# Kernel tuning notes

Hardware: AMD Instinct MI355X
Metric: run time of the kernel (lower is better)

The kernel has to match this reference:

```python
import jax, jax.numpy as jnp
import numpy as np

N, K, C, L = 8192, 12, 128, 6
FF = 4 * C
SIG_LO, SIG_HI = 1.0, 5.0
BOX = 25.0

TRI_NAMES = ("ln_g", "ln_b", "Wa", "ba", "Wga", "bga", "Wb", "bb", "Wgb", "bgb",
             "lno_g", "lno_b", "Wo", "bo", "Wgo", "bgo")
FFN_NAMES = ("ln_g", "ln_b", "W1", "b1", "W2", "b2")


def _ln(x, g, b, eps=1e-5):
    m = jnp.mean(x, axis=-1, keepdims=True)
    v = jnp.mean((x - m) ** 2, axis=-1, keepdims=True)
    return (x - m) * jax.lax.rsqrt(v + eps) * g + b


def _knn_embed(coords):
    # pairwise distances -> k smallest (self included), Gaussian RBF bank over C sigmas
    d2 = jnp.sum((coords[:, None, :] - coords[None, :, :]) ** 2, axis=-1)  # [N,N]
    dist = jnp.sqrt(jnp.maximum(d2, 0.0))
    neg_d, nbr = jax.lax.top_k(-dist, K)                      # [N,K]
    k_dist = -neg_d
    sig = jnp.linspace(SIG_LO, SIG_HI, C)                     # [C]
    g = jnp.exp(-(k_dist[..., None] ** 2) / (2.0 * sig ** 2))  # [N,K,C]
    vals = jnp.where(g > 0.1, g, 0.0)                         # threshold as in repo
    vals = jnp.where(jnp.isnan(vals), 0.0, vals)
    return nbr, vals


def _transpose_vals(v, nbr):
    # sparse rowcol_transpose: value of edge (j,i) aligned to slot of edge (i,j); 0 if absent
    n = nbr.shape[0]
    nn = nbr[nbr]                                   # [N,K,K]: neighbor lists of each neighbor j
    eq = nn == jnp.arange(n)[:, None, None]         # slot where j lists i back
    pos = jnp.argmax(eq, axis=-1)                   # [N,K]
    found = jnp.any(eq, axis=-1)                    # [N,K]
    tv = v[nbr, pos]                                # [N,K,C] value at edge (j,i)
    return jnp.where(found[..., None], tv, jnp.zeros_like(tv))


def _tri_update(v, nbr, p, incoming):
    x = _ln(v, p["ln_g"], p["ln_b"])
    a = jax.nn.sigmoid(x @ p["Wga"] + p["bga"]) * (x @ p["Wa"] + p["ba"])
    b = jax.nn.sigmoid(x @ p["Wgb"] + p["bgb"]) * (x @ p["Wb"] + p["bb"])
    if incoming:  # column/incoming update operates on transposed edges
        a = _transpose_vals(a, nbr)
        b = _transpose_vals(b, nbr)
    # sparse triangle multiplicative update over KNN neighbor slots
    k = jnp.einsum('ntc,nmtc->nmc', a, b[nbr])      # [N,K,C]
    o = _ln(k, p["lno_g"], p["lno_b"]) @ p["Wo"] + p["bo"]
    return jax.nn.sigmoid(x @ p["Wgo"] + p["bgo"]) * o


def _ffn(v, p):
    x = _ln(v, p["ln_g"], p["ln_b"])
    return jax.nn.gelu(x @ p["W1"] + p["b1"], approximate=False) @ p["W2"] + p["b2"]


def _forward(coords, tri, ffn, dec_W, dec_b):
    nbr, v = _knn_embed(coords)
    v = jax.lax.stop_gradient(v)  # embedding runs under torch.no_grad in the original

    def step(v, lp):
        tp, fp = lp
        p_row = {n: t[0] for n, t in zip(TRI_NAMES, tp)}
        p_col = {n: t[1] for n, t in zip(TRI_NAMES, tp)}
        v = v + _tri_update(v, nbr, p_row, False)   # row (outgoing) update
        v = v + _tri_update(v, nbr, p_col, True)    # col (incoming) update
        v = v + _ffn(v, dict(zip(FFN_NAMES, fp)))
        return v, None

    v, _ = jax.lax.scan(jax.checkpoint(step), v, (tri, ffn))
    s = v + _transpose_vals(v, nbr)                 # sparse_operation(edge, edge^T, op='sum')
    e = s @ dec_W + dec_b                           # [N,K,1] decode
    rows = jnp.repeat(jnp.arange(N), K)
    dense = jnp.zeros((N, N, e.shape[-1]), e.dtype)
    dense = dense.at[rows, nbr.reshape(-1)].add(e.reshape(-1, e.shape[-1]))
    return dense                                    # [N,N,1] like .to_dense()


def setup_inputs() -> dict:
    key = jax.random.key(0)
    ks = jax.random.split(key, 8)
    coords = jax.random.uniform(ks[0], (N, 3), jnp.float32) * BOX

    def lin(k, fin, fout, pre=()):
        kw, _ = jax.random.split(k)
        W = jax.random.normal(kw, pre + (fin, fout), jnp.float32) / np.sqrt(fin).astype(np.float32)
        b = jnp.zeros(pre + (fout,), jnp.float32)
        return W, b

    inp = {"coords": coords}
    k_iter = iter(jax.random.split(ks[1], 16))
    pre = (L, 2)
    inp["tri_ln_g"] = jnp.ones(pre + (C,), jnp.float32)
    inp["tri_ln_b"] = jnp.zeros(pre + (C,), jnp.float32)
    for nm in ("a", "ga", "b", "gb", "o", "go"):
        W, b = lin(next(k_iter), C, C, pre)
        inp[f"tri_W{nm}"] = W
        inp[f"tri_b{nm}"] = b
    inp["tri_lno_g"] = jnp.ones(pre + (C,), jnp.float32)
    inp["tri_lno_b"] = jnp.zeros(pre + (C,), jnp.float32)
    inp["ffn_ln_g"] = jnp.ones((L, C), jnp.float32)
    inp["ffn_ln_b"] = jnp.zeros((L, C), jnp.float32)
    inp["ffn_W1"], inp["ffn_b1"] = lin(next(k_iter), C, FF, (L,))
    inp["ffn_W2"], inp["ffn_b2"] = lin(next(k_iter), FF, C, (L,))
    inp["dec_W"], inp["dec_b"] = lin(next(k_iter), C, 1)
    return inp


def reference(coords, tri_ln_g, tri_ln_b, tri_Wa, tri_ba, tri_Wga, tri_bga,
              tri_Wb, tri_bb, tri_Wgb, tri_bgb, tri_lno_g, tri_lno_b,
              tri_Wo, tri_bo, tri_Wgo, tri_bgo,
              ffn_ln_g, ffn_ln_b, ffn_W1, ffn_b1, ffn_W2, ffn_b2,
              dec_W, dec_b):
    tri = (tri_ln_g, tri_ln_b, tri_Wa, tri_ba, tri_Wga, tri_bga,
           tri_Wb, tri_bb, tri_Wgb, tri_bgb, tri_lno_g, tri_lno_b,
           tri_Wo, tri_bo, tri_Wgo, tri_bgo)
    ffn = (ffn_ln_g, ffn_ln_b, ffn_W1, ffn_b1, ffn_W2, ffn_b2)
    return _forward(coords, tri, ffn, dec_W, dec_b)
```

## Files before the change

kernel.cpp:

```cpp
#include <hip/hip_runtime.h>
#include <hip/hip_bf16.h>
#include <stdint.h>
#include <stddef.h>

#define NPTS 8192
#define KNN  12
#define CH   128
#define FFD  512
#define MEDGE (NPTS * KNN)

typedef __attribute__((ext_vector_type(8))) _Float16 half8;
typedef __attribute__((ext_vector_type(4))) _Float16 half4;
typedef __attribute__((ext_vector_type(4))) float f32x4;

__device__ __forceinline__ float wave_sum(float v) {
#pragma unroll
  for (int off = 32; off > 0; off >>= 1) v += __shfl_xor(v, off, 64);
  return v;
}
__device__ __forceinline__ float sigm_(float x) { return 1.0f / (1.0f + expf(-x)); }
__device__ __forceinline__ float gelu_(float x) { return 0.5f * x * (1.0f + erff(x * 0.7071067811865475f)); }

__global__ __launch_bounds__(256)
void prep_coords(const float* __restrict__ c, float4* __restrict__ c4)
{
  int i = blockIdx.x * 256 + threadIdx.x;
  if (i < NPTS) c4[i] = make_float4(c[3 * i], c[3 * i + 1], c[3 * i + 2], 0.0f);
}

struct SwzArgs {
  const float* src[8];
  _Float16* dst[8];
  int K[8], N[8], B[8], perB[8];
};

__global__ __launch_bounds__(256)
void prep_weights_swz(SwzArgs sa)
{
  int g = blockIdx.y;
  int idx = blockIdx.x * 256 + threadIdx.x;
  int perB = sa.perB[g];
  if (idx >= sa.B[g] * perB) return;
  int K = sa.K[g], N = sa.N[g];
  int b = idx / perB;
  int c = idx - b * perB;
  int l16 = c & 15;
  int quad = (c >> 4) & 3;
  int rest = c >> 6;
  int kts = K >> 5;
  int kt = rest % kts;
  int mt = rest / kts;
  const float* sp = sa.src[g] + ((size_t)b * K + kt * 32 + quad * 8) * N + mt * 16 + l16;
  _Float16* dp = sa.dst[g] + ((size_t)b * perB + c) * 8;
#pragma unroll
  for (int e = 0; e < 8; ++e) dp[e] = (_Float16)sp[(size_t)e * N];
}

#define KNN_CAP 2048

__global__ __launch_bounds__(256)
void knn_embed(const float4* __restrict__ coords4, const float* __restrict__ lng,
               const float* __restrict__ lnb, int* __restrict__ nbr,
               float* __restrict__ v0, _Float16* __restrict__ xln)
{
#pragma clang fp contract(off)
  __shared__ unsigned long long buf[KNN_CAP];
  __shared__ unsigned long long sel[KNN];
  __shared__ int cnt_s;
  const int i = blockIdx.x;
  const int tid = threadIdx.x;
  const int lane = tid & 63;
  const int wv = tid >> 6;
  const float4 ci = coords4[i];

  float T2 = 9.0f;
  int cnt;
  while (true) {
    if (tid == 0) cnt_s = 0;
    __syncthreads();
    for (int j = tid; j < NPTS; j += 256) {
      float4 cj = coords4[j];
      float dx = ci.x - cj.x;
      float dy = ci.y - cj.y;
      float dz = ci.z - cj.z;
      float d2 = dx * dx + dy * dy + dz * dz;
      if (d2 < T2) {
        unsigned long long key =
            (((unsigned long long)__float_as_uint(sqrtf(d2))) << 32) | (unsigned int)j;
        int idx = atomicAdd(&cnt_s, 1);
        if (idx < KNN_CAP) buf[idx] = key;
      }
    }
    __syncthreads();
    cnt = cnt_s;
    if (cnt >= KNN) break;
    T2 *= 4.0f;
    __syncthreads();
  }
  if (cnt > KNN_CAP) cnt = KNN_CAP;

  if (wv == 0) {
    unsigned long long best[KNN];
#pragma unroll
    for (int q = 0; q < KNN; ++q) best[q] = ~0ULL;
    for (int p2 = lane; p2 < cnt; p2 += 64) {
      unsigned long long key = buf[p2];
      if (key < best[KNN - 1]) {
        best[KNN - 1] = key;
#pragma unroll
        for (int q = KNN - 2; q >= 0; --q) {
          if (best[q + 1] < best[q]) { unsigned long long t = best[q]; best[q] = best[q + 1]; best[q + 1] = t; }
        }
      }
    }
    int p = 0;
    for (int r = 0; r < KNN; ++r) {
      unsigned long long c = ~0ULL;
#pragma unroll
      for (int q = 0; q < KNN; ++q) if (q == p) c = best[q];
      unsigned long long m = c;
#pragma unroll
      for (int off = 32; off > 0; off >>= 1) {
        unsigned long long o = __shfl_xor(m, off, 64);
        if (o < m) m = o;
      }
      if (c == m) ++p;
      if (lane == 0) sel[r] = m;
    }
  }
  __syncthreads();
  if (tid < KNN) nbr[i * KNN + tid] = (int)(unsigned int)(sel[tid] & 0xFFFFFFFFULL);

  float g1 = lng[lane], g2 = lng[lane + 64];
  float bb1 = lnb[lane], bb2 = lnb[lane + 64];
  for (int k = wv * 3; k < wv * 3 + 3; ++k) {
    float d = __uint_as_float((unsigned int)(sel[k] >> 32));
    float sig1 = (float)(1.0 + 4.0 * (double)lane / 127.0);
    float sig2 = (float)(1.0 + 4.0 * (double)(lane + 64) / 127.0);
    float e1 = expf((-(d * d)) / (2.0f * sig1 * sig1));
    float e2 = expf((-(d * d)) / (2.0f * sig2 * sig2));
    float v1 = (e1 > 0.1f) ? e1 : 0.0f;
    float v2 = (e2 > 0.1f) ? e2 : 0.0f;
    size_t off = (size_t)(i * KNN + k) * CH;
    v0[off + lane] = v1;
    v0[off + lane + 64] = v2;
    float m = wave_sum(v1 + v2) * (1.0f / 128.0f);
    float d1 = v1 - m, d2 = v2 - m;
    float var = wave_sum(d1 * d1 + d2 * d2) * (1.0f / 128.0f);
    float rs = 1.0f / sqrtf(var + 1e-5f);
    xln[off + lane]      = (_Float16)(d1 * rs * g1 + bb1);
    xln[off + lane + 64] = (_Float16)(d2 * rs * g2 + bb2);
  }
}

__global__ __launch_bounds__(256)
void build_tidx(const int* __restrict__ nbr, int* __restrict__ tidx)
{
  int e = blockIdx.x * 256 + threadIdx.x;
  if (e >= MEDGE) return;
  int i = e / KNN;
  int j = nbr[e];
  int res = -1;
#pragma unroll
  for (int t = 0; t < KNN; ++t) {
    if (nbr[j * KNN + t] == i) { res = j * KNN + t; break; }
  }
  tidx[e] = res;
}

__global__ __launch_bounds__(256)
void gemm_ab_go(const _Float16* __restrict__ xln,
                const _Float16* __restrict__ wa,  const float* __restrict__ ba,
                const _Float16* __restrict__ wga, const float* __restrict__ bga,
                const _Float16* __restrict__ wb,  const float* __restrict__ bb,
                const _Float16* __restrict__ wgb, const float* __restrict__ bgb,
                const _Float16* __restrict__ wgo, const float* __restrict__ bgo,
                _Float16* __restrict__ aout, _Float16* __restrict__ bout,
                _Float16* __restrict__ gobout)
{
  const int lane = threadIdx.x & 63;
  const int quad = lane >> 4;
  const int l16 = lane & 15;
  const int gw = blockIdx.x * 4 + (threadIdx.x >> 6);
  const int base = gw * 32;
  const int chbase = quad * 16 + l16;

  half8 xf[2][4];
#pragma unroll
  for (int rt = 0; rt < 2; ++rt)
#pragma unroll
    for (int kt = 0; kt < 4; ++kt)
      xf[rt][kt] = *(const half8*)(xln + (size_t)(base + rt * 16 + l16) * CH + kt * 32 + quad * 8);

  const half8* WA  = (const half8*)wa;
  const half8* WGA = (const half8*)wga;
  const half8* WB  = (const half8*)wb;
  const half8* WGB = (const half8*)wgb;
  const half8* WGO = (const half8*)wgo;

#pragma unroll
  for (int mt = 0; mt < 8; ++mt) {
    f32x4 aA[2], aGA[2], aB[2], aGB[2], aGO[2];
    const f32x4 z = {0.f, 0.f, 0.f, 0.f};
#pragma unroll
    for (int rt = 0; rt < 2; ++rt) { aA[rt] = z; aGA[rt] = z; aB[rt] = z; aGB[rt] = z; aGO[rt] = z; }
#pragma unroll
    for (int kt = 0; kt < 4; ++kt) {
      int ch = (mt * 4 + kt) * 64 + chbase;
      half8 wfa = WA[ch], wfga = WGA[ch], wfb = WB[ch], wfgb = WGB[ch], wfgo = WGO[ch];
#pragma unroll
      for (int rt = 0; rt < 2; ++rt) {
        aA[rt]  = __builtin_amdgcn_mfma_f32_16x16x32_f16(wfa,  xf[rt][kt], aA[rt], 0, 0, 0);
        aGA[rt] = __builtin_amdgcn_mfma_f32_16x16x32_f16(wfga, xf[rt][kt], aGA[rt], 0, 0, 0);
        aB[rt]  = __builtin_amdgcn_mfma_f32_16x16x32_f16(wfb,  xf[rt][kt], aB[rt], 0, 0, 0);
        aGB[rt] = __builtin_amdgcn_mfma_f32_16x16x32_f16(wfgb, xf[rt][kt], aGB[rt], 0, 0, 0);
        aGO[rt] = __builtin_amdgcn_mfma_f32_16x16x32_f16(wfgo, xf[rt][kt], aGO[rt], 0, 0, 0);
      }
    }
    f32x4 bva  = *(const f32x4*)(ba  + mt * 16 + quad * 4);
    f32x4 bvga = *(const f32x4*)(bga + mt * 16 + quad * 4);
    f32x4 bvb  = *(const f32x4*)(bb  + mt * 16 + quad * 4);
    f32x4 bvgb = *(const f32x4*)(bgb + mt * 16 + quad * 4);
    f32x4 bvgo = *(const f32x4*)(bgo + mt * 16 + quad * 4);
#pragma unroll
    for (int rt = 0; rt < 2; ++rt) {
      half4 av, bv, gv;
#pragma unroll
      for (int r = 0; r < 4; ++r) {
        av[r] = (_Float16)(sigm_(aGA[rt][r] + bvga[r]) * (aA[rt][r] + bva[r]));
        bv[r] = (_Float16)(sigm_(aGB[rt][r] + bvgb[r]) * (aB[rt][r] + bvb[r]));
        gv[r] = (_Float16)(sigm_(aGO[rt][r] + bvgo[r]));
      }
      size_t off = (size_t)(base + rt * 16 + l16) * CH + mt * 16 + quad * 4;
      *(half4*)(aout + off) = av;
      *(half4*)(bout + off) = bv;
      *(half4*)(gobout + off) = gv;
    }
  }
}

__global__ __launch_bounds__(192)
void tri_einsum_ln(const _Float16* __restrict__ a, const _Float16* __restrict__ b,
                   const int* __restrict__ nbr, const int* __restrict__ tidx,
                   const float* __restrict__ lng, const float* __restrict__ lnb,
                   _Float16* __restrict__ kout, int incoming)
{
  __shared__ float As[KNN][CH];
  __shared__ int bidx[KNN][KNN];
  __shared__ int nbr_s[KNN];
  const int n = blockIdx.x;
  const int tid = threadIdx.x;
  if (tid < KNN) nbr_s[tid] = nbr[n * KNN + tid];
  __syncthreads();
  if (tid < KNN * KNN) {
    int m = tid / KNN, t = tid - m * KNN;
    int j = nbr_s[m];
    bidx[m][t] = incoming ? tidx[j * KNN + t] : (j * KNN + t);
  }
  for (int idx = tid; idx < KNN * CH; idx += 192) {
    int t = idx >> 7, c = idx & 127;
    float av;
    if (incoming) {
      int ti = tidx[n * KNN + t];
      av = (ti >= 0) ? (float)(a[(size_t)ti * CH + c]) : 0.0f;
    } else {
      av = (float)(a[(size_t)(n * KNN + t) * CH + c]);
    }
    As[t][c] = av;
  }
  __syncthreads();

  const int m = tid >> 4;
  const int c8 = (tid & 15) * 8;
  float acc[8];
#pragma unroll
  for (int r = 0; r < 8; ++r) acc[r] = 0.0f;
#pragma unroll
  for (int t = 0; t < KNN; ++t) {
    int bi = bidx[m][t];
    if (bi >= 0) {
      half8 bv = *(const half8*)(b + (size_t)bi * CH + c8);
      f32x4 a0 = *(const f32x4*)&As[t][c8];
      f32x4 a1 = *(const f32x4*)&As[t][c8 + 4];
#pragma unroll
      for (int r = 0; r < 4; ++r) acc[r] += a0[r] * (float)bv[r];
#pragma unroll
      for (int r = 0; r < 4; ++r) acc[4 + r] += a1[r] * (float)bv[4 + r];
    }
  }
  float s = 0.0f, sq = 0.0f;
#pragma unroll
  for (int r = 0; r < 8; ++r) { s += acc[r]; sq += acc[r] * acc[r]; }
#pragma unroll
  for (int off = 1; off < 16; off <<= 1) {
    s += __shfl_xor(s, off, 64);
    sq += __shfl_xor(sq, off, 64);
  }
  float mean = s * (1.0f / 128.0f);
  float var = sq * (1.0f / 128.0f) - mean * mean;
  if (var < 0.0f) var = 0.0f;
  float rs = 1.0f / sqrtf(var + 1e-5f);
  half8 o;
#pragma unroll
  for (int r = 0; r < 8; ++r)
    o[r] = (_Float16)((acc[r] - mean) * rs * lng[c8 + r] + lnb[c8 + r]);
  *(half8*)(kout + (size_t)(n * KNN + m) * CH + c8) = o;
}

__global__ __launch_bounds__(256)
void og_gemm(const _Float16* __restrict__ kln,
             const _Float16* __restrict__ wo,  const float* __restrict__ bo,
             const _Float16* __restrict__ gob, float* __restrict__ v,
             const float* __restrict__ nlng, const float* __restrict__ nlnb,
             _Float16* __restrict__ xlnN)
{
  const int lane = threadIdx.x & 63;
  const int quad = lane >> 4;
  const int l16 = lane & 15;
  const int gw = blockIdx.x * 4 + (threadIdx.x >> 6);
  const int base = gw * 16;
  const int chbase = quad * 16 + l16;
  const size_t rowOff = (size_t)(base + l16) * CH;

  half8 kf[4];
#pragma unroll
  for (int kt = 0; kt < 4; ++kt)
    kf[kt] = *(const half8*)(kln + rowOff + kt * 32 + quad * 8);

  const half8* WO = (const half8*)wo;
  f32x4 vn[8];
  float s = 0.0f, sq = 0.0f;
#pragma unroll
  for (int mt = 0; mt < 8; ++mt) {
    f32x4 acc = {0.f, 0.f, 0.f, 0.f};
#pragma unroll
    for (int kt = 0; kt < 4; ++kt)
      acc = __builtin_amdgcn_mfma_f32_16x16x32_f16(WO[(mt * 4 + kt) * 64 + chbase], kf[kt], acc, 0, 0, 0);
    half4 g4 = *(const half4*)(gob + rowOff + mt * 16 + quad * 4);
    f32x4 bo4 = *(const f32x4*)(bo + mt * 16 + quad * 4);
    f32x4 vv = *(const f32x4*)(v + rowOff + mt * 16 + quad * 4);
#pragma unroll
    for (int r = 0; r < 4; ++r) {
      float nv = vv[r] + (float)g4[r] * (acc[r] + bo4[r]);
      vn[mt][r] = nv;
      s += nv;
      sq += nv * nv;
    }
    *(f32x4*)(v + rowOff + mt * 16 + quad * 4) = vn[mt];
  }
  s  += __shfl_xor(s, 16, 64);  s  += __shfl_xor(s, 32, 64);
  sq += __shfl_xor(sq, 16, 64); sq += __shfl_xor(sq, 32, 64);
  float mean = s * (1.0f / 128.0f);
  float var = sq * (1.0f / 128.0f) - mean * mean;
  if (var < 0.0f) var = 0.0f;
  float rs = 1.0f / sqrtf(var + 1e-5f);
#pragma unroll
  for (int mt = 0; mt < 8; ++mt) {
    f32x4 g4 = *(const f32x4*)(nlng + mt * 16 + quad * 4);
    f32x4 b4 = *(const f32x4*)(nlnb + mt * 16 + quad * 4);
    half4 o;
#pragma unroll
    for (int r = 0; r < 4; ++r)
      o[r] = (_Float16)((vn[mt][r] - mean) * rs * g4[r] + b4[r]);
    *(half4*)(xlnN + rowOff + mt * 16 + quad * 4) = o;
  }
}

#define HADDR(row, ch) ((((row) * 64 + ((ch) ^ ((row) & 7)))) * 8)

__global__ __launch_bounds__(256)
void ffn_fused(const _Float16* __restrict__ xln,
               const _Float16* __restrict__ w1, const float* __restrict__ b1,
               const _Float16* __restrict__ w2, const float* __restrict__ b2,
               float* __restrict__ v,
               const float* __restrict__ nlng, const float* __restrict__ nlnb,
               _Float16* __restrict__ xlnN)
{
  __shared__ alignas(16) _Float16 hlds[32 * FFD];
  __shared__ float part[32][4][2];
  const int tid = threadIdx.x;
  const int lane = tid & 63;
  const int w = tid >> 6;
  const int quad = lane >> 4;
  const int l16 = lane & 15;
  const int rowBase = blockIdx.x * 32;
  const int chbase = quad * 16 + l16;

  half8 xf[2][4];
#pragma unroll
  for (int rt = 0; rt < 2; ++rt)
#pragma unroll
    for (int kt = 0; kt < 4; ++kt)
      xf[rt][kt] = *(const half8*)(xln + (size_t)(rowBase + rt * 16 + l16) * CH + kt * 32 + quad * 8);

  const half8* W1 = (const half8*)w1;
#pragma unroll
  for (int mt = 0; mt < 8; ++mt) {
    int mtg = w * 8 + mt;
    f32x4 acc[2];
    const f32x4 z = {0.f, 0.f, 0.f, 0.f};
    acc[0] = z; acc[1] = z;
#pragma unroll
    for (int kt = 0; kt < 4; ++kt) {
      half8 wf = W1[(mtg * 4 + kt) * 64 + chbase];
#pragma unroll
      for (int rt = 0; rt < 2; ++rt)
        acc[rt] = __builtin_amdgcn_mfma_f32_16x16x32_f16(wf, xf[rt][kt], acc[rt], 0, 0, 0);
    }
    f32x4 bv = *(const f32x4*)(b1 + mtg * 16 + quad * 4);
    int ch = mtg * 2 + (quad >> 1);
    int sub = (quad & 1) * 4;
#pragma unroll
    for (int rt = 0; rt < 2; ++rt) {
      int row = rt * 16 + l16;
      half4 hh;
#pragma unroll
      for (int r = 0; r < 4; ++r)
        hh[r] = (_Float16)(gelu_(acc[rt][r] + bv[r]));
      *(half4*)&hlds[HADDR(row, ch) + sub] = hh;
    }
  }
  __syncthreads();

  const half8* W2 = (const half8*)w2;
  f32x4 vn2[2][2];
  float s2[2] = {0.f, 0.f}, q2[2] = {0.f, 0.f};
#pragma unroll
  for (int m2 = 0; m2 < 2; ++m2) {
    int mt = w * 2 + m2;
    f32x4 accA[2], accB[2];
    const f32x4 z = {0.f, 0.f, 0.f, 0.f};
    accA[0] = z; accA[1] = z; accB[0] = z; accB[1] = z;
#pragma unroll
    for (int kt = 0; kt < 16; kt += 2) {
      half8 wf0 = W2[(mt * 16 + kt) * 64 + chbase];
      half8 wf1 = W2[(mt * 16 + kt + 1) * 64 + chbase];
#pragma unroll
      for (int rt = 0; rt < 2; ++rt) {
        int row = rt * 16 + l16;
        half8 hf0 = *(const half8*)&hlds[HADDR(row, kt * 4 + quad)];
        half8 hf1 = *(const half8*)&hlds[HADDR(row, (kt + 1) * 4 + quad)];
        accA[rt] = __builtin_amdgcn_mfma_f32_16x16x32_f16(wf0, hf0, accA[rt], 0, 0, 0);
        accB[rt] = __builtin_amdgcn_mfma_f32_16x16x32_f16(wf1, hf1, accB[rt], 0, 0, 0);
      }
    }
    f32x4 bv = *(const f32x4*)(b2 + mt * 16 + quad * 4);
#pragma unroll
    for (int rt = 0; rt < 2; ++rt) {
      size_t off = (size_t)(rowBase + rt * 16 + l16) * CH + mt * 16 + quad * 4;
      f32x4 vv = *(const f32x4*)(v + off);
#pragma unroll
      for (int r = 0; r < 4; ++r) {
        float nv = vv[r] + accA[rt][r] + accB[rt][r] + bv[r];
        vn2[m2][rt][r] = nv;
        s2[rt] += nv;
        q2[rt] += nv * nv;
      }
      *(f32x4*)(v + off) = vn2[m2][rt];
    }
  }
#pragma unroll
  for (int rt = 0; rt < 2; ++rt) {
    float ss = s2[rt], qq = q2[rt];
    ss += __shfl_xor(ss, 16, 64); ss += __shfl_xor(ss, 32, 64);
    qq += __shfl_xor(qq, 16, 64); qq += __shfl_xor(qq, 32, 64);
    if (quad == 0) { part[rt * 16 + l16][w][0] = ss; part[rt * 16 + l16][w][1] = qq; }
  }
  __syncthreads();
#pragma unroll
  for (int rt = 0; rt < 2; ++rt) {
    int row = rt * 16 + l16;
    float su = part[row][0][0] + part[row][1][0] + part[row][2][0] + part[row][3][0];
    float qu = part[row][0][1] + part[row][1][1] + part[row][2][1] + part[row][3][1];
    float mean = su * (1.0f / 128.0f);
    float var = qu * (1.0f / 128.0f) - mean * mean;
    if (var < 0.0f) var = 0.0f;
    float rs = 1.0f / sqrtf(var + 1e-5f);
#pragma unroll
    for (int m2 = 0; m2 < 2; ++m2) {
      int mt = w * 2 + m2;
      f32x4 g4 = *(const f32x4*)(nlng + mt * 16 + quad * 4);
      f32x4 b4 = *(const f32x4*)(nlnb + mt * 16 + quad * 4);
      half4 o;
#pragma unroll
      for (int r = 0; r < 4; ++r)
        o[r] = (_Float16)((vn2[m2][rt][r] - mean) * rs * g4[r] + b4[r]);
      *(half4*)(xlnN + (size_t)(rowBase + row) * CH + mt * 16 + quad * 4) = o;
    }
  }
}

__global__ __launch_bounds__(256)
void decode_row(const float* __restrict__ vin, const int* __restrict__ tidx,
                const int* __restrict__ nbr, const float* __restrict__ decW,
                const float* __restrict__ decB, float* __restrict__ out)
{
  __shared__ float ev[KNN];
  __shared__ int nbr_s[KNN];
  const int n = blockIdx.x;
  const int tid = threadIdx.x;
  const int lane = tid & 63;
  const int w = tid >> 6;
  if (tid < KNN) nbr_s[tid] = nbr[n * KNN + tid];
  float dw1 = decW[lane], dw2 = decW[lane + 64];
  for (int k = w; k < KNN; k += 4) {
    int e = n * KNN + k;
    int ti = tidx[e];
    float s1 = vin[(size_t)e * CH + lane];
    float s2 = vin[(size_t)e * CH + 64 + lane];
    if (ti >= 0) {
      s1 += vin[(size_t)ti * CH + lane];
      s2 += vin[(size_t)ti * CH + 64 + lane];
    }
    float tot = wave_sum(s1 * dw1 + s2 * dw2);
    if (lane == 0) ev[k] = tot + decB[0];
  }
  __syncthreads();
  float4 z = make_float4(0.f, 0.f, 0.f, 0.f);
  float4* row = (float4*)(out + (size_t)n * NPTS);
  for (int idx = tid; idx < NPTS / 4; idx += 256) row[idx] = z;
  __syncthreads();
  if (tid < KNN) out[(size_t)n * NPTS + nbr_s[tid]] = ev[tid];
}

extern "C" void kernel_launch(void* const* d_in, const int* in_sizes, int n_in,
                              void* d_out, int out_size, void* d_ws, size_t ws_size,
                              hipStream_t stream)
{
  (void)in_sizes; (void)n_in; (void)out_size; (void)ws_size;
  const float* coords  = (const float*)d_in[0];
  const float* t_ln_g  = (const float*)d_in[1];
  const float* t_ln_b  = (const float*)d_in[2];
  const float* t_Wa    = (const float*)d_in[3];
  const float* t_ba    = (const float*)d_in[4];
  const float* t_Wga   = (const float*)d_in[5];
  const float* t_bga   = (const float*)d_in[6];
  const float* t_Wb    = (const float*)d_in[7];
  const float* t_bb    = (const float*)d_in[8];
  const float* t_Wgb   = (const float*)d_in[9];
  const float* t_bgb   = (const float*)d_in[10];
  const float* t_Wo    = (const float*)d_in[11];
  const float* t_bo    = (const float*)d_in[12];
  const float* t_Wgo   = (const float*)d_in[13];
  const float* t_bgo   = (const float*)d_in[14];
  const float* t_lno_g = (const float*)d_in[15];
  const float* t_lno_b = (const float*)d_in[16];
  const float* f_ln_g  = (const float*)d_in[17];
  const float* f_ln_b  = (const float*)d_in[18];
  const float* f_W1    = (const float*)d_in[19];
  const float* f_b1    = (const float*)d_in[20];
  const float* f_W2    = (const float*)d_in[21];
  const float* f_b2    = (const float*)d_in[22];
  const float* dec_W   = (const float*)d_in[23];
  const float* dec_b   = (const float*)d_in[24];

  const size_t NKC = (size_t)MEDGE * CH;
  char* ws = (char*)d_ws;
  float* v        = (float*)(ws);
  _Float16* kln   = (_Float16*)(ws + NKC * 4);
  _Float16* gx    = (_Float16*)(ws + NKC * 6);
  int* nbr        = (int*)(ws + NKC * 8);
  int* tidx       = (int*)(ws + NKC * 8 + (size_t)MEDGE * 4);
  float4* coords4 = (float4*)(ws + NKC * 8 + (size_t)MEDGE * 8);
  _Float16* wbase = (_Float16*)(ws + NKC * 8 + (size_t)MEDGE * 8 + NPTS * 16);
  const size_t TRIH = (size_t)12 * 2048 * 8;
  _Float16* wA  = wbase;
  _Float16* wGA = wA  + TRIH;
  _Float16* wB  = wGA + TRIH;
  _Float16* wGB = wB  + TRIH;
  _Float16* wGO = wGB + TRIH;
  _Float16* wO  = wGO + TRIH;
  _Float16* w1  = wO  + TRIH;
  _Float16* w2  = w1  + (size_t)6 * 8192 * 8;

  _Float16* abuf = (_Float16*)d_out;
  _Float16* bbuf = abuf + NKC;

  prep_coords<<<32, 256, 0, stream>>>(coords, coords4);

  SwzArgs sa;
  sa.src[0] = t_Wa;  sa.dst[0] = wA;  sa.K[0] = CH;  sa.N[0] = CH;  sa.B[0] = 12; sa.perB[0] = 2048;
  sa.src[1] = t_Wga; sa.dst[1] = wGA; sa.K[1] = CH;  sa.N[1] = CH;  sa.B[1] = 12; sa.perB[1] = 2048;
  sa.src[2] = t_Wb;  sa.dst[2] = wB;  sa.K[2] = CH;  sa.N[2] = CH;  sa.B[2] = 12; sa.perB[2] = 2048;
  sa.src[3] = t_Wgb; sa.dst[3] = wGB; sa.K[3] = CH;  sa.N[3] = CH;  sa.B[3] = 12; sa.perB[3] = 2048;
  sa.src[4] = t_Wgo; sa.dst[4] = wGO; sa.K[4] = CH;  sa.N[4] = CH;  sa.B[4] = 12; sa.perB[4] = 2048;
  sa.src[5] = t_Wo;  sa.dst[5] = wO;  sa.K[5] = CH;  sa.N[5] = CH;  sa.B[5] = 12; sa.perB[5] = 2048;
  sa.src[6] = f_W1;  sa.dst[6] = w1;  sa.K[6] = CH;  sa.N[6] = FFD; sa.B[6] = 6;  sa.perB[6] = 8192;
  sa.src[7] = f_W2;  sa.dst[7] = w2;  sa.K[7] = FFD; sa.N[7] = CH;  sa.B[7] = 6;  sa.perB[7] = 8192;
  dim3 pgrid(192, 8);
  prep_weights_swz<<<pgrid, 256, 0, stream>>>(sa);

  knn_embed<<<NPTS, 256, 0, stream>>>(coords4, t_ln_g, t_ln_b, nbr, v, gx);
  build_tidx<<<MEDGE / 256, 256, 0, stream>>>(nbr, tidx);

  const size_t WS = (size_t)2048 * 8;
  gemm_ab_go<<<MEDGE / 128, 256, 0, stream>>>(gx,
      wA, t_ba, wGA, t_bga, wB, t_bb, wGB, t_bgb, wGO, t_bgo,
      abuf, bbuf, gx);

  for (int l = 0; l < 6; ++l) {
    int s0 = 2 * l, s1 = 2 * l + 1, s2 = 2 * l + 2;
    tri_einsum_ln<<<NPTS, 192, 0, stream>>>(abuf, bbuf, nbr, tidx,
        t_lno_g + s0 * CH, t_lno_b + s0 * CH, kln, 0);
    og_gemm<<<MEDGE / 64, 256, 0, stream>>>(kln,
        wO + s0 * WS, t_bo + s0 * CH, gx, v,
        t_ln_g + s1 * CH, t_ln_b + s1 * CH, gx);
    gemm_ab_go<<<MEDGE / 128, 256, 0, stream>>>(gx,
        wA + s1 * WS, t_ba + s1 * CH, wGA + s1 * WS, t_bga + s1 * CH,
        wB + s1 * WS, t_bb + s1 * CH, wGB + s1 * WS, t_bgb + s1 * CH,
        wGO + s1 * WS, t_bgo + s1 * CH,
        abuf, bbuf, gx);
    tri_einsum_ln<<<NPTS, 192, 0, stream>>>(abuf, bbuf, nbr, tidx,
        t_lno_g + s1 * CH, t_lno_b + s1 * CH, kln, 1);
    og_gemm<<<MEDGE / 64, 256, 0, stream>>>(kln,
        wO + s1 * WS, t_bo + s1 * CH, gx, v,
        f_ln_g + l * CH, f_ln_b + l * CH, gx);
    const float* ng = (l < 5) ? (t_ln_g + s2 * CH) : t_ln_g;
    const float* nb = (l < 5) ? (t_ln_b + s2 * CH) : t_ln_b;
    ffn_fused<<<MEDGE / 32, 256, 0, stream>>>(gx,
        w1 + (size_t)l * 8192 * 8, f_b1 + l * FFD,
        w2 + (size_t)l * 8192 * 8, f_b2 + l * CH,
        v, ng, nb, gx);
    if (l < 5) {
      gemm_ab_go<<<MEDGE / 128, 256, 0, stream>>>(gx,
          wA + s2 * WS, t_ba + s2 * CH, wGA + s2 * WS, t_bga + s2 * CH,
          wB + s2 * WS, t_bb + s2 * CH, wGB + s2 * WS, t_bgb + s2 * CH,
          wGO + s2 * WS, t_bgo + s2 * CH,
          abuf, bbuf, gx);
    }
  }

  decode_row<<<NPTS, 256, 0, stream>>>(v, tidx, nbr, dec_W, dec_b, (float*)d_out);
}
```

Measured before the change: 2.611 ms.

## Fuse triangle einsum+LN with output gated GEMM via LDS staging

Merges the sparse triangle einsum/LayerNorm kernel with the output projection/gating GEMM. Each block now handles 4 points (48 edge rows) and keeps the normalized triangle result in LDS instead of writing it to and rereading it from a global buffer. The A operand is staged in LDS as fp16 with 16-byte vector loads instead of scalar fp32. The trade-off is that 192-thread blocks give 3 MFMA waves for the GEMM stage instead of 4 per block, and more LDS per block may reduce occupancy.

Result: no change. 2.563 ms (-1.8%).

```diff
diff --git a/kernel.cpp b/kernel.cpp
--- a/kernel.cpp
+++ b/kernel.cpp
@@ -240,92 +240,97 @@
 }
 
 __global__ __launch_bounds__(192)
-void tri_einsum_ln(const _Float16* __restrict__ a, const _Float16* __restrict__ b,
-                   const int* __restrict__ nbr, const int* __restrict__ tidx,
-                   const float* __restrict__ lng, const float* __restrict__ lnb,
-                   _Float16* __restrict__ kout, int incoming)
-{
-  __shared__ float As[KNN][CH];
-  __shared__ int bidx[KNN][KNN];
-  __shared__ int nbr_s[KNN];
-  const int n = blockIdx.x;
+void tri_og(const _Float16* __restrict__ a, const _Float16* __restrict__ b,
+            const int* __restrict__ nbr, const int* __restrict__ tidx,
+            const float* __restrict__ lng, const float* __restrict__ lnb,
+            const _Float16* __restrict__ wo, const float* __restrict__ bo,
+            const _Float16* __restrict__ gob, float* __restrict__ v,
+            const float* __restrict__ nlng, const float* __restrict__ nlnb,
+            _Float16* __restrict__ xlnN, int incoming)
+{
+  __shared__ alignas(16) _Float16 As[48][136];
+  __shared__ alignas(16) _Float16 klds[48][136];
+  __shared__ int bidx[4][KNN][KNN];
+  __shared__ int nbr_s[4][KNN];
+  const int n0 = blockIdx.x * 4;
   const int tid = threadIdx.x;
-  if (tid < KNN) nbr_s[tid] = nbr[n * KNN + tid];
-  __syncthreads();
-  if (tid < KNN * KNN) {
-    int m = tid / KNN, t = tid - m * KNN;
-    int j = nbr_s[m];
-    bidx[m][t] = incoming ? tidx[j * KNN + t] : (j * KNN + t);
-  }
-  for (int idx = tid; idx < KNN * CH; idx += 192) {
-    int t = idx >> 7, c = idx & 127;
-    float av;
+
+  if (tid < 48) nbr_s[tid / KNN][tid % KNN] = nbr[n0 * KNN + tid];
+  __syncthreads();
+  for (int it = tid; it < 4 * KNN * KNN; it += 192) {
+    int nn = it / (KNN * KNN);
+    int r = it - nn * KNN * KNN;
+    int m = r / KNN, t = r - m * KNN;
+    int j = nbr_s[nn][m];
+    bidx[nn][m][t] = incoming ? tidx[j * KNN + t] : (j * KNN + t);
+  }
+  for (int it = tid; it < 4 * KNN * 16; it += 192) {
+    int nn = it / (KNN * 16);
+    int r = it - nn * (KNN * 16);
+    int t = r >> 4;
+    int c8 = (r & 15) * 8;
+    half8 av;
     if (incoming) {
-      int ti = tidx[n * KNN + t];
-      av = (ti >= 0) ? (float)(a[(size_t)ti * CH + c]) : 0.0f;
+      int ti = tidx[(size_t)(n0 + nn) * KNN + t];
+      if (ti >= 0) av = *(const half8*)(a + (size_t)ti * CH + c8);
+      else {
+#pragma unroll
+        for (int e = 0; e < 8; ++e) av[e] = (_Float16)0.0f;
+      }
     } else {
-      av = (float)(a[(size_t)(n * KNN + t) * CH + c]);
-    }
-    As[t][c] = av;
-  }
-  __syncthreads();
-
-  const int m = tid >> 4;
+      av = *(const half8*)(a + (size_t)((n0 + nn) * KNN + t) * CH + c8);
+    }
+    *(half8*)&As[nn * KNN + t][c8] = av;
+  }
+  __syncthreads();
+
+  const int m2 = tid >> 4;
   const int c8 = (tid & 15) * 8;
-  float acc[8];
-#pragma unroll
-  for (int r = 0; r < 8; ++r) acc[r] = 0.0f;
-#pragma unroll
-  for (int t = 0; t < KNN; ++t) {
-    int bi = bidx[m][t];
-    if (bi >= 0) {
-      half8 bv = *(const half8*)(b + (size_t)bi * CH + c8);
-      f32x4 a0 = *(const f32x4*)&As[t][c8];
-      f32x4 a1 = *(const f32x4*)&As[t][c8 + 4];
-#pragma unroll
-      for (int r = 0; r < 4; ++r) acc[r] += a0[r] * (float)bv[r];
-#pragma unroll
-      for (int r = 0; r < 4; ++r) acc[4 + r] += a1[r] * (float)bv[4 + r];
-    }
-  }
-  float s = 0.0f, sq = 0.0f;
-#pragma unroll
-  for (int r = 0; r < 8; ++r) { s += acc[r]; sq += acc[r] * acc[r]; }
-#pragma unroll
-  for (int off = 1; off < 16; off <<= 1) {
-    s += __shfl_xor(s, off, 64);
-    sq += __shfl_xor(sq, off, 64);
-  }
-  float mean = s * (1.0f / 128.0f);
-  float var = sq * (1.0f / 128.0f) - mean * mean;
-  if (var < 0.0f) var = 0.0f;
-  float rs = 1.0f / sqrtf(var + 1e-5f);
-  half8 o;
-#pragma unroll
-  for (int r = 0; r < 8; ++r)
-    o[r] = (_Float16)((acc[r] - mean) * rs * lng[c8 + r] + lnb[c8 + r]);
-  *(half8*)(kout + (size_t)(n * KNN + m) * CH + c8) = o;
-}
-
-__global__ __launch_bounds__(256)
-void og_gemm(const _Float16* __restrict__ kln,
-             const _Float16* __restrict__ wo,  const float* __restrict__ bo,
-             const _Float16* __restrict__ gob, float* __restrict__ v,
-             const float* __restrict__ nlng, const float* __restrict__ nlnb,
-             _Float16* __restrict__ xlnN)
-{
-  const int lane = threadIdx.x & 63;
+  for (int nn = 0; nn < 4; ++nn) {
+    float acc[8];
+#pragma unroll
+    for (int r = 0; r < 8; ++r) acc[r] = 0.0f;
+#pragma unroll
+    for (int t = 0; t < KNN; ++t) {
+      int bi = bidx[nn][m2][t];
+      if (bi >= 0) {
+        half8 bv = *(const half8*)(b + (size_t)bi * CH + c8);
+        half8 av = *(const half8*)&As[nn * KNN + t][c8];
+#pragma unroll
+        for (int r = 0; r < 8; ++r) acc[r] += (float)av[r] * (float)bv[r];
+      }
+    }
+    float s = 0.0f, sq = 0.0f;
+#pragma unroll
+    for (int r = 0; r < 8; ++r) { s += acc[r]; sq += acc[r] * acc[r]; }
+#pragma unroll
+    for (int off = 1; off < 16; off <<= 1) {
+      s += __shfl_xor(s, off, 64);
+      sq += __shfl_xor(sq, off, 64);
+    }
+    float mean = s * (1.0f / 128.0f);
+    float var = sq * (1.0f / 128.0f) - mean * mean;
+    if (var < 0.0f) var = 0.0f;
+    float rs = 1.0f / sqrtf(var + 1e-5f);
+    half8 o;
+#pragma unroll
+    for (int r = 0; r < 8; ++r)
+      o[r] = (_Float16)((acc[r] - mean) * rs * lng[c8 + r] + lnb[c8 + r]);
+    *(half8*)&klds[nn * KNN + m2][c8] = o;
+  }
+  __syncthreads();
+
+  const int lane = tid & 63;
+  const int w = tid >> 6;
   const int quad = lane >> 4;
   const int l16 = lane & 15;
-  const int gw = blockIdx.x * 4 + (threadIdx.x >> 6);
-  const int base = gw * 16;
   const int chbase = quad * 16 + l16;
-  const size_t rowOff = (size_t)(base + l16) * CH;
+  const size_t rowOff = (size_t)(blockIdx.x * 48 + w * 16 + l16) * CH;
 
   half8 kf[4];
 #pragma unroll
   for (int kt = 0; kt < 4; ++kt)
-    kf[kt] = *(const half8*)(kln + rowOff + kt * 32 + quad * 8);
+    kf[kt] = *(const half8*)&klds[w * 16 + l16][kt * 32 + quad * 8];
 
   const half8* WO = (const half8*)wo;
   f32x4 vn[8];
@@ -557,7 +562,6 @@
   const size_t NKC = (size_t)MEDGE * CH;
   char* ws = (char*)d_ws;
   float* v        = (float*)(ws);
-  _Float16* kln   = (_Float16*)(ws + NKC * 4);
   _Float16* gx    = (_Float16*)(ws + NKC * 6);
   int* nbr        = (int*)(ws + NKC * 8);
   int* tidx       = (int*)(ws + NKC * 8 + (size_t)MEDGE * 4);
@@ -600,21 +604,19 @@
 
   for (int l = 0; l < 6; ++l) {
     int s0 = 2 * l, s1 = 2 * l + 1, s2 = 2 * l + 2;
-    tri_einsum_ln<<<NPTS, 192, 0, stream>>>(abuf, bbuf, nbr, tidx,
-        t_lno_g + s0 * CH, t_lno_b + s0 * CH, kln, 0);
-    og_gemm<<<MEDGE / 64, 256, 0, stream>>>(kln,
+    tri_og<<<NPTS / 4, 192, 0, stream>>>(abuf, bbuf, nbr, tidx,
+        t_lno_g + s0 * CH, t_lno_b + s0 * CH,
         wO + s0 * WS, t_bo + s0 * CH, gx, v,
-        t_ln_g + s1 * CH, t_ln_b + s1 * CH, gx);
+        t_ln_g + s1 * CH, t_ln_b + s1 * CH, gx, 0);
     gemm_ab_go<<<MEDGE / 128, 256, 0, stream>>>(gx,
         wA + s1 * WS, t_ba + s1 * CH, wGA + s1 * WS, t_bga + s1 * CH,
         wB + s1 * WS, t_bb + s1 * CH, wGB + s1 * WS, t_bgb + s1 * CH,
         wGO + s1 * WS, t_bgo + s1 * CH,
         abuf, bbuf, gx);
-    tri_einsum_ln<<<NPTS, 192, 0, stream>>>(abuf, bbuf, nbr, tidx,
-        t_lno_g + s1 * CH, t_lno_b + s1 * CH, kln, 1);
-    og_gemm<<<MEDGE / 64, 256, 0, stream>>>(kln,
+    tri_og<<<NPTS / 4, 192, 0, stream>>>(abuf, bbuf, nbr, tidx,
+        t_lno_g + s1 * CH, t_lno_b + s1 * CH,
         wO + s1 * WS, t_bo + s1 * CH, gx, v,
-        f_ln_g + l * CH, f_ln_b + l * CH, gx);
+        f_ln_g + l * CH, f_ln_b + l * CH, gx, 1);
     const float* ng = (l < 5) ? (t_ln_g + s2 * CH) : t_ln_g;
     const float* nb = (l < 5) ? (t_ln_b + s2 * CH) : t_ln_b;
     ffn_fused<<<MEDGE / 32, 256, 0, stream>>>(gx,
```
